# Performance work log

Hardware: AMD Instinct MI355X
Metric: run time of the kernel (lower is better)

## Reference

```python
import jax, jax.numpy as jnp
import numpy as np
import math

B, C, IMG, E, H, L, FF, D, NCLS = 4, 3, 64, 256, 8, 512, 4, 4, 1000
N = IMG * IMG  # 4096 pixel tokens
HS = H * E    # head_size = embedding_size * heads (per original code)


def setup_inputs() -> dict:
    key = jax.random.key(0)
    ks = jax.random.split(key, 32)
    s = 0.02
    nrm = lambda k, shape: (jax.random.normal(k, shape, jnp.float32) * s)
    inp = {
        "x": jax.random.normal(ks[0], (B, C, N), jnp.float32),
        "conv_w": nrm(ks[1], (E, C)),                 # 1x1 conv1d kernel
        "conv_b": jnp.zeros((E,), jnp.float32),
        "pos_emb": nrm(ks[2], (N, E)),
        "latents": jax.random.normal(ks[3], (L, E), jnp.float32),
        # cross-attention (queries from latents, keys/values from image tokens)
        "ca_wq": nrm(ks[4], (E, HS)),
        "ca_wk": nrm(ks[5], (E, HS)),
        "ca_wv": nrm(ks[6], (E, HS)),
        "ca_wu": nrm(ks[7], (HS, E)),
        "ca_bu": jnp.zeros((E,), jnp.float32),
        "ca_ln_g": jnp.ones((E,), jnp.float32),
        "ca_ln_b": jnp.zeros((E,), jnp.float32),
        # transformer blocks, stacked along depth for lax.scan
        "blk_wq": nrm(ks[8], (D, E, HS)),
        "blk_wk": nrm(ks[9], (D, E, HS)),
        "blk_wv": nrm(ks[10], (D, E, HS)),
        "blk_wu": nrm(ks[11], (D, HS, E)),
        "blk_bu": jnp.zeros((D, E), jnp.float32),
        "blk_ln1_g": jnp.ones((D, E), jnp.float32),
        "blk_ln1_b": jnp.zeros((D, E), jnp.float32),
        "blk_w1": nrm(ks[12], (D, E, FF * E)),
        "blk_b1": jnp.zeros((D, FF * E), jnp.float32),
        "blk_w2": nrm(ks[13], (D, FF * E, E)),
        "blk_b2": jnp.zeros((D, E), jnp.float32),
        "blk_ln2_g": jnp.ones((D, E), jnp.float32),
        "blk_ln2_b": jnp.zeros((D, E), jnp.float32),
        "cls_w": nrm(ks[14], (E, NCLS)),
        "cls_b": jnp.zeros((NCLS,), jnp.float32),
        "heads": H,
    }
    return inp


def _ln(x, g, b):
    m = jnp.mean(x, axis=-1, keepdims=True)
    v = jnp.mean(jnp.square(x - m), axis=-1, keepdims=True)
    return g * (x - m) * jax.lax.rsqrt(v + 1e-5) + b


def _mha(q_in, kv_in, wq, wk, wv, wu, bu, heads):
    # Faithful to original: each head has dim = embedding_size (head_size = heads*emb),
    # and the scale is sqrt(emb // heads).
    b, nq, e = q_in.shape
    nk = kv_in.shape[1]
    q = (q_in @ wq).reshape(b, nq, heads, e)
    k = (kv_in @ wk).reshape(b, nk, heads, e)
    v = (kv_in @ wv).reshape(b, nk, heads, e)
    scale = 1.0 / math.sqrt(e // heads)
    w = jax.nn.softmax(jnp.einsum('bqhe,bkhe->bhqk', q, k) * scale, axis=-1)
    a = jnp.einsum('bhqk,bkhe->bqhe', w, v).reshape(b, nq, heads * e)
    return a @ wu + bu


def reference(x, conv_w, conv_b, pos_emb, latents,
              ca_wq, ca_wk, ca_wv, ca_wu, ca_bu, ca_ln_g, ca_ln_b,
              blk_wq, blk_wk, blk_wv, blk_wu, blk_bu,
              blk_ln1_g, blk_ln1_b, blk_w1, blk_b1, blk_w2, blk_b2,
              blk_ln2_g, blk_ln2_b, cls_w, cls_b, heads):
    bsz = x.shape[0]
    # 1x1 conv1d over flattened pixels: (B, C, N) -> (B, N, E), plus positions
    tokens = jnp.einsum('bcn,ec->bne', x, conv_w) + conv_b + pos_emb
    # latents as queries, image tokens as keys/values (cross-attention)
    z = jnp.broadcast_to(latents, (bsz,) + latents.shape)
    z = _ln(_mha(z, tokens, ca_wq, ca_wk, ca_wv, ca_wu, ca_bu, heads) + z,
            ca_ln_g, ca_ln_b)
    # dropout is identity in eval mode

    def block(z, p):
        wq, wk, wv, wu, bu, g1, b1, w1, c1, w2, c2, g2, b2 = p
        z = _ln(_mha(z, z, wq, wk, wv, wu, bu, heads) + z, g1, b1)
        h = jax.nn.gelu(z @ w1 + c1, approximate=False) @ w2 + c2
        z = _ln(h + z, g2, b2)
        return z, None

    z, _ = jax.lax.scan(block, z,
                        (blk_wq, blk_wk, blk_wv, blk_wu, blk_bu,
                         blk_ln1_g, blk_ln1_b, blk_w1, blk_b1,
                         blk_w2, blk_b2, blk_ln2_g, blk_ln2_b))
    # global average over latents, then classifier
    return jnp.mean(z, axis=1) @ cls_w + cls_b
```

## Files before the change

### kernel.cpp

```cpp
#include <hip/hip_runtime.h>
#include <hip/hip_bf16.h>
#include <math.h>


typedef __attribute__((ext_vector_type(8))) short s8v;
typedef __attribute__((ext_vector_type(4))) float f32x4;
typedef __attribute__((ext_vector_type(16))) float f32x16;
typedef __attribute__((ext_vector_type(4))) unsigned u32x4;

__device__ __forceinline__ short f2b(float f) {
  union { float f; unsigned u; } a; a.f = f;
  unsigned r = a.u + 0x7fff + ((a.u >> 16) & 1);
  return (short)(r >> 16);
}
__device__ __forceinline__ float b2f(short s) {
  union { unsigned u; float f; } a; a.u = ((unsigned)(unsigned short)s) << 16;
  return a.f;
}
__device__ __forceinline__ unsigned cvtpk(float lo, float hi) {
  unsigned r;
  asm("v_cvt_pk_bf16_f32 %0, %1, %2" : "=v"(r) : "v"(lo), "v"(hi));
  return r;
}

__device__ __forceinline__ void gl16(const void* gp, void* lp) {
  __builtin_amdgcn_global_load_lds(
      (const __attribute__((address_space(1))) unsigned int*)gp,
      (__attribute__((address_space(3))) unsigned int*)lp, 16, 0, 0);
}

__global__ __launch_bounds__(256) void k_tokens(
    const float* __restrict__ x, const float* __restrict__ cw,
    const float* __restrict__ cb, const float* __restrict__ pe,
    short* __restrict__ tok)
{
  int idx = blockIdx.x * 256 + threadIdx.x;
  int e = idx & 255;
  int n = (idx >> 8) & 4095;
  int b = idx >> 20;
  float s = cb[e] + pe[n * 256 + e];
#pragma unroll
  for (int c = 0; c < 3; ++c)
    s += x[b * 12288 + c * 4096 + n] * cw[e * 3 + c];
  tok[idx] = f2b(s);
}

template<typename TI>
__global__ __launch_bounds__(256) void k_tr(
    const TI* __restrict__ in, short* __restrict__ out,
    int R, int C, long sIn, long sOut)
{
  __shared__ float t[32][33];
  const TI* ib = in + (long)blockIdx.z * sIn;
  short* ob = out + (long)blockIdx.z * sOut;
  int c0 = blockIdx.x * 32, r0 = blockIdx.y * 32;
  int tx = threadIdx.x & 31, ty = threadIdx.x >> 5;
#pragma unroll
  for (int i = 0; i < 4; ++i)
    t[ty * 4 + i][tx] = (float)ib[(long)(r0 + ty * 4 + i) * C + c0 + tx];
  __syncthreads();
#pragma unroll
  for (int i = 0; i < 4; ++i)
    ob[(long)(c0 + ty * 4 + i) * R + r0 + tx] = f2b(t[tx][ty * 4 + i]);
}

struct TrJob {
  const float* src; short* dst;
  int R, C; long sIn, sOut;
  int mode, tilesPerZ, z, tileBase;
  float scale;
};
struct TrJobs { TrJob j[11]; };

__global__ __launch_bounds__(256) void k_trbatch(TrJobs jb, int njobs)
{
  __shared__ float t[32][33];
  int tb = blockIdx.x, ji = 0;
#pragma unroll
  for (int k = 1; k < 11; ++k)
    if (k < njobs && tb >= jb.j[k].tileBase) ji = k;
  TrJob J = jb.j[ji];
  int local = tb - J.tileBase;
  if (J.mode == 1) {
    long o = (long)local * 8192 + threadIdx.x;
#pragma unroll
    for (int k = 0; k < 32; ++k)
      J.dst[o + k * 256] = f2b(J.src[o + k * 256] * J.scale);
    return;
  }
  int zi = local / J.tilesPerZ, ti = local - zi * J.tilesPerZ;
  int ntx = J.C >> 5;
  int tx = ti % ntx, ty = ti / ntx;
  const float* ib = J.src + (long)zi * J.sIn;
  short* ob = J.dst + (long)zi * J.sOut;
  int c0 = tx * 32, r0 = ty * 32;
  int lx = threadIdx.x & 31, ly = threadIdx.x >> 5;
#pragma unroll
  for (int i = 0; i < 4; ++i)
    t[ly * 4 + i][lx] = ib[(long)(r0 + ly * 4 + i) * J.C + c0 + lx];
  __syncthreads();
#pragma unroll
  for (int i = 0; i < 4; ++i)
    ob[(long)(c0 + ly * 4 + i) * J.R + r0 + lx] = f2b(t[lx][ly * 4 + i] * J.scale);
}

template<int EPI>
__global__ __launch_bounds__(256) void k_mgemm(
    const short* __restrict__ A, const short* __restrict__ Bt,
    void* __restrict__ Cv, const float* __restrict__ bias,
    int K, int lda, int ldb, int ldc,
    long sA, long sB, long sC, int zdA, int zmA, int zdB, int zmB)
{
  __shared__ char As[8192];
  __shared__ char Bs[8192];
  int z = blockIdx.z;
  const short* Ab = A + ((long)((z / zdA) % zmA)) * sA;
  const short* Bb = Bt + ((long)((z / zdB) % zmB)) * sB;
  int t = threadIdx.x;
  int lane = t & 63, w = t >> 6;
  int wr = w >> 1, wc = w & 1;
  int g = lane >> 4, l15 = lane & 15;
  long row0 = (long)blockIdx.y * 128, col0 = (long)blockIdx.x * 128;
  const f32x4 zz = {0.f, 0.f, 0.f, 0.f};
  f32x4 acc[4][4];
#pragma unroll
  for (int m = 0; m < 4; ++m)
#pragma unroll
    for (int n = 0; n < 4; ++n) acc[m][n] = zz;

  auto mload = [&](s8v* aa, s8v* bb, int kk) {
#pragma unroll
    for (int i = 0; i < 2; ++i) {
      int r = i * 64 + (t >> 2), c = t & 3;
      aa[i] = *(const s8v*)&Ab[(row0 + r) * (long)lda + kk + c * 8];
      bb[i] = *(const s8v*)&Bb[(col0 + r) * (long)ldb + kk + c * 8];
    }
  };
  auto mstore = [&](s8v* aa, s8v* bb) {
#pragma unroll
    for (int i = 0; i < 2; ++i) {
      int r = i * 64 + (t >> 2), c = t & 3;
      int off = (r * 64 + c * 16) ^ ((r & 7) << 4);
      *(s8v*)&As[off] = aa[i];
      *(s8v*)&Bs[off] = bb[i];
    }
  };
  auto mcomp = [&]() {
    s8v af[4], bfr[4];
#pragma unroll
    for (int m = 0; m < 4; ++m) {
      int r = wr * 64 + m * 16 + l15;
      af[m] = *(const s8v*)&As[(r * 64 + g * 16) ^ ((r & 7) << 4)];
    }
#pragma unroll
    for (int n = 0; n < 4; ++n) {
      int r = wc * 64 + n * 16 + l15;
      bfr[n] = *(const s8v*)&Bs[(r * 64 + g * 16) ^ ((r & 7) << 4)];
    }
#pragma unroll
    for (int m = 0; m < 4; ++m)
#pragma unroll
      for (int n = 0; n < 4; ++n)
        acc[m][n] = __builtin_amdgcn_mfma_f32_16x16x32_bf16(af[m], bfr[n], acc[m][n], 0, 0, 0);
  };

  s8v a0[2], b0[2], a1[2], b1[2];
  mload(a0, b0, 0);
  for (int k0 = 0; k0 < K; k0 += 64) {
    __syncthreads(); mstore(a0, b0); __syncthreads();
    mload(a1, b1, k0 + 32);
    mcomp();
    __syncthreads(); mstore(a1, b1); __syncthreads();
    if (k0 + 64 < K) mload(a0, b0, k0 + 64);
    mcomp();
  }

  long zo = (long)z * sC;
#pragma unroll
  for (int m = 0; m < 4; ++m)
#pragma unroll
    for (int n = 0; n < 4; ++n)
#pragma unroll
      for (int r = 0; r < 4; ++r) {
        long rr = row0 + wr * 64 + m * 16 + g * 4 + r;
        long cc = col0 + wc * 64 + n * 16 + l15;
        float v = acc[m][n][r];
        if (EPI == 1) {
          v += bias[cc];
          v = 0.5f * v * (1.f + erff(v * 0.70710678118654752f));
        }
        if (EPI == 2)
          ((float*)Cv)[zo + rr * ldc + cc] = v;
        else
          ((short*)Cv)[zo + rr * ldc + cc] = f2b(v);
      }
}

__global__ __launch_bounds__(512, 2) void k_mflash5(
    const short* __restrict__ Qp, const short* __restrict__ Kp,
    const short* __restrict__ Vtp, short* __restrict__ Opart,
    float* __restrict__ MLp,
    int nk, int ldq, int ldk, int ldvt,
    long qh, long qb, long kh, long kb, long vh, long vb)
{
  __shared__ char pool[131072];
  int t = threadIdx.x, lane = t & 63, w = t >> 6;
  int l31 = lane & 31, hi = lane >> 5;
  int h = blockIdx.y, b = blockIdx.z;
  int kv = blockIdx.x & 3, qblk = blockIdx.x >> 2;
  const short* Q  = Qp  + (long)h * qh + (long)b * qb;
  const short* Kg = Kp  + (long)h * kh + (long)b * kb;
  const short* Vg = Vtp + (long)h * vh + (long)b * vb;
  int q0w = qblk * 256 + w * 32;
  int nkq = nk >> 2;
  int NIT = nkq >> 6;
  long k0 = (long)kv * nkq;

  s8v qf[16];
  {
    const short* Qrow = Q + (long)(q0w + l31) * ldq + hi * 8;
#pragma unroll
    for (int s = 0; s < 16; ++s) qf[s] = *(const s8v*)(Qrow + s * 16);
  }

  const char* KgB = (const char*)Kg;
  const char* VgB = (const char*)Vg;
  unsigned koff[4], voff[4];
#pragma unroll
  for (int c = 0; c < 4; ++c) {
    int r = 8 * w + 2 * c + hi;
    koff[c] = (unsigned)((k0 + r) * (long)ldk * 2) + ((l31 ^ (r & 31)) << 4);
    int rv = 32 * w + 8 * c + (lane >> 3);
    voff[c] = (unsigned)(((long)rv * ldvt + k0) * 2) + (((lane & 7) ^ (lane >> 3)) << 4);
  }
  const unsigned kStep = (unsigned)(64 * ldk * 2);

  auto stage = [&](int bsel) {
    char* kd = pool + bsel * 65536 + (w << 12);
    char* vd = kd + 32768;
#pragma unroll
    for (int c = 0; c < 4; ++c) { gl16(KgB + koff[c], kd + c * 1024); koff[c] += kStep; }
#pragma unroll
    for (int c = 0; c < 4; ++c) { gl16(VgB + voff[c], vd + c * 1024); voff[c] += 128; }
  };

  f32x16 accO[8];
#pragma unroll
  for (int n = 0; n < 8; ++n)
#pragma unroll
    for (int i = 0; i < 16; ++i) accO[n][i] = 0.f;
  float mrow = -1e30f, lrow = 0.f;

  stage(0);

  for (int it = 0; it < NIT; ++it) {
    int cur = it & 1;
    asm volatile("s_waitcnt vmcnt(0)" ::: "memory");
    __syncthreads();
    if (it + 1 < NIT) stage(cur ^ 1);
    const char* kls = pool + cur * 65536;
    const char* vls = kls + 32768;

    f32x16 sacc[2];
#pragma unroll
    for (int i = 0; i < 16; ++i) { sacc[0][i] = 0.f; sacc[1][i] = 0.f; }
    __builtin_amdgcn_s_setprio(1);
#pragma unroll
    for (int tt = 0; tt < 2; ++tt) {
      int r = tt * 32 + l31;
#pragma unroll
      for (int s = 0; s < 16; ++s) {
        s8v kf = *(const s8v*)&kls[r * 512 + (((2 * s + hi) ^ l31) << 4)];
        sacc[tt] = __builtin_amdgcn_mfma_f32_32x32x16_bf16(kf, qf[s], sacc[tt], 0, 0, 0);
      }
    }
    __builtin_amdgcn_s_setprio(0);

    float mt = sacc[0][0];
#pragma unroll
    for (int i = 1; i < 16; ++i) mt = fmaxf(mt, sacc[0][i]);
#pragma unroll
    for (int i = 0; i < 16; ++i) mt = fmaxf(mt, sacc[1][i]);
    mt = fmaxf(mt, __shfl_xor(mt, 32));
    if (__any(mt - mrow > 8.f)) {
      float mn = fmaxf(mrow, mt);
      float al = __expf(mrow - mn);
      mrow = mn; lrow *= al;
#pragma unroll
      for (int r = 0; r < 16; ++r) {
        float alr = __shfl(al, (r & 3) + 8 * (r >> 2) + 4 * hi);
#pragma unroll
        for (int n = 0; n < 8; ++n) accO[n][r] *= alr;
      }
    }
    float ls = 0.f;
#pragma unroll
    for (int tt = 0; tt < 2; ++tt)
#pragma unroll
      for (int i = 0; i < 16; ++i) {
        float p = __expf(sacc[tt][i] - mrow);
        sacc[tt][i] = p; ls += p;
      }
    ls += __shfl_xor(ls, 32);
    lrow += ls;

    s8v pa[4];
#pragma unroll
    for (int s = 0; s < 4; ++s) {
      int tt = s >> 1, r0 = (s & 1) * 8;
      unsigned w0 = cvtpk(sacc[tt][r0 + 0], sacc[tt][r0 + 1]);
      unsigned w1 = cvtpk(sacc[tt][r0 + 2], sacc[tt][r0 + 3]);
      unsigned w2 = cvtpk(sacc[tt][r0 + 4], sacc[tt][r0 + 5]);
      unsigned w3 = cvtpk(sacc[tt][r0 + 6], sacc[tt][r0 + 7]);
      unsigned x0 = (unsigned)__shfl_xor((int)w0, 32);
      unsigned x1 = (unsigned)__shfl_xor((int)w1, 32);
      unsigned x2 = (unsigned)__shfl_xor((int)w2, 32);
      unsigned x3 = (unsigned)__shfl_xor((int)w3, 32);
      u32x4 pw;
      pw.x = hi ? x2 : w0;
      pw.y = hi ? x3 : w1;
      pw.z = hi ? w2 : x0;
      pw.w = hi ? w3 : x1;
      pa[s] = *(s8v*)&pw;
    }

    __builtin_amdgcn_s_setprio(1);
#pragma unroll
    for (int n = 0; n < 8; ++n) {
      int rv = n * 32 + l31;
#pragma unroll
      for (int s2 = 0; s2 < 4; ++s2) {
        s8v vf = *(const s8v*)&vls[rv * 128 + (((2 * s2 + hi) ^ (l31 & 7)) << 4)];
        accO[n] = __builtin_amdgcn_mfma_f32_32x32x16_bf16(pa[s2], vf, accO[n], 0, 0, 0);
      }
    }
    __builtin_amdgcn_s_setprio(0);
  }

  long prow = (((long)kv * 4 + b) * 8 + h) * 512;
  short* Ob = Opart + prow * 256;
  float* MLb = MLp + prow * 2;
  if (lane < 32) {
    MLb[(q0w + l31) * 2] = mrow;
    MLb[(q0w + l31) * 2 + 1] = lrow;
  }
#pragma unroll
  for (int n = 0; n < 8; ++n)
#pragma unroll
    for (int r = 0; r < 16; ++r) {
      int q = q0w + (r & 3) + 8 * (r >> 2) + 4 * hi;
      Ob[(long)q * 256 + n * 32 + l31] = f2b(accO[n][r]);
    }
}

__global__ __launch_bounds__(512) void k_fcomb(
    const short* __restrict__ Op, const float* __restrict__ ML,
    short* __restrict__ O)
{
  int d = threadIdx.x & 255;
  int q = blockIdx.x * 2 + (threadIdx.x >> 8);
  int h = blockIdx.y, b = blockIdx.z;
  const long kvs = 4L * 8 * 512;
  long r0 = ((long)b * 8 + h) * 512 + q;
  float mm[4], ll[4], m = -1e30f;
#pragma unroll
  for (int kv = 0; kv < 4; ++kv) {
    mm[kv] = ML[(kv * kvs + r0) * 2];
    ll[kv] = ML[(kv * kvs + r0) * 2 + 1];
    m = fmaxf(m, mm[kv]);
  }
  float wv[4], lsum = 0.f;
#pragma unroll
  for (int kv = 0; kv < 4; ++kv) { wv[kv] = __expf(mm[kv] - m); lsum += ll[kv] * wv[kv]; }
  float inv = 1.f / lsum, acc = 0.f;
#pragma unroll
  for (int kv = 0; kv < 4; ++kv)
    acc += b2f(Op[(kv * kvs + r0) * 256 + d]) * wv[kv];
  O[(long)b * 1048576 + (long)q * 2048 + h * 256 + d] = f2b(acc * inv);
}

__global__ __launch_bounds__(256) void k_bias_res_ln(
    const float* __restrict__ Yp, int nPart, long pStride,
    const float* __restrict__ bias,
    const float* __restrict__ res, int resMod,
    const float* __restrict__ g, const float* __restrict__ bta,
    float* __restrict__ out, short* __restrict__ out_bf)
{
  __shared__ float red[4];
  int row = blockIdx.x, e = threadIdx.x;
  float v = bias[e] + res[(long)(row % resMod) * 256 + e];
  for (int s = 0; s < nPart; ++s) v += Yp[s * pStride + (long)row * 256 + e];
  float s1 = v;
#pragma unroll
  for (int o = 32; o > 0; o >>= 1) s1 += __shfl_down(s1, o);
  if ((e & 63) == 0) red[e >> 6] = s1;
  __syncthreads();
  float mean = (red[0] + red[1] + red[2] + red[3]) * (1.f / 256.f);
  float d = v - mean;
  __syncthreads();
  float s2 = d * d;
#pragma unroll
  for (int o = 32; o > 0; o >>= 1) s2 += __shfl_down(s2, o);
  if ((e & 63) == 0) red[e >> 6] = s2;
  __syncthreads();
  float var = (red[0] + red[1] + red[2] + red[3]) * (1.f / 256.f);
  float o = g[e] * d * rsqrtf(var + 1e-5f) + bta[e];
  out[(long)row * 256 + e] = o;
  out_bf[(long)row * 256 + e] = f2b(o);
}

__global__ __launch_bounds__(256) void k_meancls(
    const float* __restrict__ z, const float* __restrict__ w,
    const float* __restrict__ bias, float* __restrict__ out)
{
  __shared__ float zms[256];
  int b = blockIdx.y, e = threadIdx.x;
  float s = 0.f;
  for (int l = 0; l < 512; ++l) s += z[((long)b * 512 + l) * 256 + e];
  zms[e] = s * (1.f / 512.f);
  __syncthreads();
  int j = blockIdx.x * 256 + e;
  if (j >= 1000) return;
  float acc = bias[j];
  for (int e2 = 0; e2 < 256; ++e2) acc += zms[e2] * w[e2 * 1000 + j];
  out[b * 1000 + j] = acc;
}

extern "C" void kernel_launch(void* const* d_in, const int* in_sizes, int n_in,
                              void* d_out, int out_size, void* d_ws, size_t ws_size,
                              hipStream_t stream)
{
  (void)in_sizes; (void)n_in; (void)out_size; (void)ws_size;
  const float* x       = (const float*)d_in[0];
  const float* conv_w  = (const float*)d_in[1];
  const float* conv_b  = (const float*)d_in[2];
  const float* pos_emb = (const float*)d_in[3];
  const float* latents = (const float*)d_in[4];
  const float* ca_wq   = (const float*)d_in[5];
  const float* ca_wk   = (const float*)d_in[6];
  const float* ca_wv   = (const float*)d_in[7];
  const float* ca_wu   = (const float*)d_in[8];
  const float* ca_bu   = (const float*)d_in[9];
  const float* ca_ln_g = (const float*)d_in[10];
  const float* ca_ln_b = (const float*)d_in[11];
  const float* blk_wq  = (const float*)d_in[12];
  const float* blk_wk  = (const float*)d_in[13];
  const float* blk_wv  = (const float*)d_in[14];
  const float* blk_wu  = (const float*)d_in[15];
  const float* blk_bu  = (const float*)d_in[16];
  const float* blk_ln1_g = (const float*)d_in[17];
  const float* blk_ln1_b = (const float*)d_in[18];
  const float* blk_w1  = (const float*)d_in[19];
  const float* blk_b1  = (const float*)d_in[20];
  const float* blk_w2  = (const float*)d_in[21];
  const float* blk_b2  = (const float*)d_in[22];
  const float* blk_ln2_g = (const float*)d_in[23];
  const float* blk_ln2_b = (const float*)d_in[24];
  const float* cls_w   = (const float*)d_in[25];
  const float* cls_b   = (const float*)d_in[26];
  float* out = (float*)d_out;

  short* wqT_ca = (short*)d_ws;
  short* wkT_ca = wqT_ca + 524288;
  short* wuT_ca = wkT_ca + 524288;
  short* wv_ca  = wuT_ca + 524288;
  short* lat_bf = wv_ca + 524288;
  short* wqkT   = lat_bf + 131072;
  short* wvT    = wqkT + 4194304;
  short* wuT_b  = wvT + 2097152;
  short* w1T    = wuT_b + 2097152;
  short* w2T    = w1T + 1048576;
  short* tok_bf = w2T + 1048576;
  short* tokT   = tok_bf + 4194304;
  short* qCA    = tokT + 4194304;
  short* qtil   = qCA + 1048576;
  short* MstT   = qtil + 1048576;
  short* VtB    = MstT + 524288;
  short* bufO   = VtB + 4194304;
  short* h1     = bufO + 4194304;
  short* z_bf   = h1 + 2097152;
  float* z      = (float*)(z_bf + 524288);
  float* zm     = z + 524288;
  float* Ypart  = zm + 1024;
  short* Opart  = (short*)(Ypart + 4194304);
  float* MLp    = (float*)(Opart + 16777216);
  short* QKb    = tok_bf;

  const float scale = 0.17677669529663687f;
  const int BIG = 1 << 30;

  TrJobs JB; int nj = 0, base = 0;
  auto addT = [&](const float* s, short* d, int R, int C, long sIn, long sOut,
                  int zc, float sc) {
    int tpz = (C >> 5) * (R >> 5);
    JB.j[nj] = {s, d, R, C, sIn, sOut, 0, tpz, zc, base, sc};
    base += tpz * zc; ++nj;
  };
  auto addC = [&](const float* s, short* d, int nelem) {
    int tpz = nelem >> 13;
    JB.j[nj] = {s, d, 0, 0, 0, 0, 1, tpz, 1, base, 1.f};
    base += tpz; ++nj;
  };
  addT(ca_wq, wqT_ca, 256, 2048, 0, 0, 1, scale);
  addT(ca_wk, wkT_ca, 256, 2048, 0, 0, 1, 1.f);
  addT(ca_wu, wuT_ca, 2048, 256, 0, 0, 1, 1.f);
  addT(blk_wq, wqkT, 256, 2048, 524288, 1048576, 4, scale);
  addT(blk_wk, wqkT + 524288, 256, 2048, 524288, 1048576, 4, 1.f);
  addT(blk_wv, wvT, 256, 2048, 524288, 524288, 4, 1.f);
  addT(blk_wu, wuT_b, 2048, 256, 524288, 524288, 4, 1.f);
  addT(blk_w1, w1T, 256, 1024, 262144, 262144, 4, 1.f);
  addT(blk_w2, w2T, 1024, 256, 262144, 262144, 4, 1.f);
  addC(ca_wv, wv_ca, 524288);
  addC(latents, lat_bf, 131072);
  k_trbatch<<<base, 256, 0, stream>>>(JB, nj);

  k_tokens<<<16384, 256, 0, stream>>>(x, conv_w, conv_b, pos_emb, tok_bf);
  k_tr<__hip_bfloat16><<<dim3(8, 128, 4), 256, 0, stream>>>(
      (const __hip_bfloat16*)tok_bf, tokT, 4096, 256, 1048576, 1048576);

  k_mgemm<0><<<dim3(16, 4, 1), 256, 0, stream>>>(
      lat_bf, wqT_ca, qCA, nullptr, 256, 256, 256, 2048, 0, 0, 0, 1, BIG, 1, BIG);
  k_mgemm<0><<<dim3(2, 4, 8), 256, 0, stream>>>(
      qCA, wkT_ca, qtil, nullptr, 256, 2048, 256, 256, 256, 65536, 131072, 1, 8, 1, 8);
  k_mgemm<0><<<dim3(2, 2, 8), 256, 0, stream>>>(
      wuT_ca, wv_ca, MstT, nullptr, 256, 2048, 2048, 2048, 256, 256, 256, 1, 8, 1, 8);
  k_mflash5<<<dim3(8, 8, 4), 512, 0, stream>>>(
      qtil, tok_bf, tokT, Opart, MLp, 4096, 256, 256, 4096,
      131072L, 0L, 0L, 1048576L, 0L, 1048576L);
  k_fcomb<<<dim3(256, 8, 4), 512, 0, stream>>>(Opart, MLp, bufO);
  k_mgemm<2><<<dim3(2, 16, 8), 256, 0, stream>>>(
      bufO, MstT, Ypart, nullptr, 256, 2048, 2048, 256, 256, 256, 524288, 1, 8, 1, 8);
  k_bias_res_ln<<<2048, 256, 0, stream>>>(Ypart, 8, 524288L, ca_bu, latents, 512,
                                          ca_ln_g, ca_ln_b, z, z_bf);

  for (int d = 0; d < 4; ++d) {
    k_mgemm<0><<<dim3(32, 16, 1), 256, 0, stream>>>(
        z_bf, wqkT + (long)d * 1048576, QKb, nullptr,
        256, 256, 256, 4096, 0, 0, 0, 1, BIG, 1, BIG);
    k_mgemm<0><<<dim3(4, 2, 32), 256, 0, stream>>>(
        wvT + (long)d * 524288, z_bf, VtB, nullptr,
        256, 256, 256, 512, 65536, 131072, 131072, 1, 8, 8, BIG);
    k_mflash5<<<dim3(8, 8, 4), 512, 0, stream>>>(
        QKb, QKb + 2048, VtB, Opart, MLp, 512, 4096, 4096, 512,
        256L, 2097152L, 256L, 2097152L, 131072L, 1048576L);
    k_fcomb<<<dim3(256, 8, 4), 512, 0, stream>>>(Opart, MLp, bufO);
    k_mgemm<2><<<dim3(2, 16, 8), 256, 0, stream>>>(
        bufO, wuT_b + (long)d * 524288, Ypart, nullptr,
        256, 2048, 2048, 256, 256, 256, 524288, 1, 8, 1, 8);
    k_bias_res_ln<<<2048, 256, 0, stream>>>(Ypart, 8, 524288L, blk_bu + d * 256, z, 2048,
        blk_ln1_g + d * 256, blk_ln1_b + d * 256, z, z_bf);
    k_mgemm<1><<<dim3(8, 16, 1), 256, 0, stream>>>(
        z_bf, w1T + (long)d * 262144, h1, blk_b1 + d * 1024,
        256, 256, 256, 1024, 0, 0, 0, 1, BIG, 1, BIG);
    k_mgemm<2><<<dim3(2, 16, 8), 256, 0, stream>>>(
        h1, w2T + (long)d * 262144, Ypart, nullptr,
        128, 1024, 1024, 256, 128, 128, 524288, 1, 8, 1, 8);
    k_bias_res_ln<<<2048, 256, 0, stream>>>(Ypart, 8, 524288L, blk_b2 + d * 256, z, 2048,
        blk_ln2_g + d * 256, blk_ln2_b + d * 256, z, z_bf);
  }

  k_meancls<<<dim3(4, 4), 256, 0, stream>>>(z, cls_w, cls_b, out);
}
```

Before: 635.7 us.

## Batch GEMMs into multi-job launches, fuse token transpose, refine flash waits

Replaces the templated GEMM with a job-table kernel so independent GEMMs (QK and V projections, cross-attention weight products) share one launch. Token embedding now writes both the row-major and the transposed copy, which removes a separate transpose kernel. The cross-attention Wq·Wk product is now computed from weights first, dropping the latent Q projection. The flash kernel uses partial vmcnt waits plus an extra barrier so K loads overlap the softmax. The epilogue mode becomes a runtime branch, and the transposed token stores are uncoalesced strided writes.

```diff
diff --git a/kernel.cpp b/kernel.cpp
--- a/kernel.cpp
+++ b/kernel.cpp
@@ -29,39 +29,27 @@
       (__attribute__((address_space(3))) unsigned int*)lp, 16, 0, 0);
 }
 
-__global__ __launch_bounds__(256) void k_tokens(
+__global__ __launch_bounds__(256) void k_tokens2(
     const float* __restrict__ x, const float* __restrict__ cw,
     const float* __restrict__ cb, const float* __restrict__ pe,
-    short* __restrict__ tok)
-{
-  int idx = blockIdx.x * 256 + threadIdx.x;
-  int e = idx & 255;
-  int n = (idx >> 8) & 4095;
-  int b = idx >> 20;
-  float s = cb[e] + pe[n * 256 + e];
-#pragma unroll
-  for (int c = 0; c < 3; ++c)
-    s += x[b * 12288 + c * 4096 + n] * cw[e * 3 + c];
-  tok[idx] = f2b(s);
-}
-
-template<typename TI>
-__global__ __launch_bounds__(256) void k_tr(
-    const TI* __restrict__ in, short* __restrict__ out,
-    int R, int C, long sIn, long sOut)
-{
-  __shared__ float t[32][33];
-  const TI* ib = in + (long)blockIdx.z * sIn;
-  short* ob = out + (long)blockIdx.z * sOut;
-  int c0 = blockIdx.x * 32, r0 = blockIdx.y * 32;
-  int tx = threadIdx.x & 31, ty = threadIdx.x >> 5;
-#pragma unroll
-  for (int i = 0; i < 4; ++i)
-    t[ty * 4 + i][tx] = (float)ib[(long)(r0 + ty * 4 + i) * C + c0 + tx];
-  __syncthreads();
-#pragma unroll
-  for (int i = 0; i < 4; ++i)
-    ob[(long)(c0 + ty * 4 + i) * R + r0 + tx] = f2b(t[tx][ty * 4 + i]);
+    short* __restrict__ tok, short* __restrict__ tokT)
+{
+  int b = blockIdx.y, n0 = blockIdx.x * 32;
+  int e = threadIdx.x;
+  float c0 = cw[e * 3], c1 = cw[e * 3 + 1], c2 = cw[e * 3 + 2], cbv = cb[e];
+  const float* xb = x + b * 12288 + n0;
+  short acc[32];
+#pragma unroll
+  for (int i = 0; i < 32; ++i) {
+    int n = n0 + i;
+    float s = cbv + pe[n * 256 + e] + xb[i] * c0 + xb[4096 + i] * c1 + xb[8192 + i] * c2;
+    short v = f2b(s);
+    tok[((long)b * 4096 + n) * 256 + e] = v;
+    acc[i] = v;
+  }
+  short* tr = tokT + ((long)b * 256 + e) * 4096 + n0;
+#pragma unroll
+  for (int i = 0; i < 32; ++i) tr[i] = acc[i];
 }
 
 struct TrJob {
@@ -104,23 +92,35 @@
     ob[(long)(c0 + ly * 4 + i) * J.R + r0 + lx] = f2b(t[lx][ly * 4 + i] * J.scale);
 }
 
-template<int EPI>
-__global__ __launch_bounds__(256) void k_mgemm(
-    const short* __restrict__ A, const short* __restrict__ Bt,
-    void* __restrict__ Cv, const float* __restrict__ bias,
-    int K, int lda, int ldb, int ldc,
-    long sA, long sB, long sC, int zdA, int zmA, int zdB, int zmB)
+struct GJob {
+  const short* A; const short* Bt; void* C; const float* bias;
+  int K, lda, ldb, ldc;
+  long sA, sB, sC;
+  int zdA, zmA, zdB, zmB;
+  int epi, gx, gy, blockBase;
+};
+struct GJobs { GJob j[4]; };
+
+__global__ __launch_bounds__(256) void k_gemm_m(GJobs jb, int njobs)
 {
   __shared__ char As[8192];
   __shared__ char Bs[8192];
-  int z = blockIdx.z;
-  const short* Ab = A + ((long)((z / zdA) % zmA)) * sA;
-  const short* Bb = Bt + ((long)((z / zdB) % zmB)) * sB;
+  int bid = blockIdx.x, ji = 0;
+#pragma unroll
+  for (int k = 1; k < 4; ++k)
+    if (k < njobs && bid >= jb.j[k].blockBase) ji = k;
+  GJob J = jb.j[ji];
+  int local = bid - J.blockBase;
+  int bx = local % J.gx, rest = local / J.gx;
+  int by = rest % J.gy, bz = rest / J.gy;
+  const short* Ab = J.A + ((long)((bz / J.zdA) % J.zmA)) * J.sA;
+  const short* Bb = J.Bt + ((long)((bz / J.zdB) % J.zmB)) * J.sB;
+  int lda = J.lda, ldb = J.ldb;
   int t = threadIdx.x;
   int lane = t & 63, w = t >> 6;
   int wr = w >> 1, wc = w & 1;
   int g = lane >> 4, l15 = lane & 15;
-  long row0 = (long)blockIdx.y * 128, col0 = (long)blockIdx.x * 128;
+  long row0 = (long)by * 128, col0 = (long)bx * 128;
   const f32x4 zz = {0.f, 0.f, 0.f, 0.f};
   f32x4 acc[4][4];
 #pragma unroll
@@ -166,16 +166,16 @@
 
   s8v a0[2], b0[2], a1[2], b1[2];
   mload(a0, b0, 0);
-  for (int k0 = 0; k0 < K; k0 += 64) {
+  for (int k0 = 0; k0 < J.K; k0 += 64) {
     __syncthreads(); mstore(a0, b0); __syncthreads();
     mload(a1, b1, k0 + 32);
     mcomp();
     __syncthreads(); mstore(a1, b1); __syncthreads();
-    if (k0 + 64 < K) mload(a0, b0, k0 + 64);
+    if (k0 + 64 < J.K) mload(a0, b0, k0 + 64);
     mcomp();
   }
 
-  long zo = (long)z * sC;
+  long zo = (long)bz * J.sC;
 #pragma unroll
   for (int m = 0; m < 4; ++m)
 #pragma unroll
@@ -185,18 +185,18 @@
         long rr = row0 + wr * 64 + m * 16 + g * 4 + r;
         long cc = col0 + wc * 64 + n * 16 + l15;
         float v = acc[m][n][r];
-        if (EPI == 1) {
-          v += bias[cc];
+        if (J.epi == 1) {
+          v += J.bias[cc];
           v = 0.5f * v * (1.f + erff(v * 0.70710678118654752f));
         }
-        if (EPI == 2)
-          ((float*)Cv)[zo + rr * ldc + cc] = v;
+        if (J.epi == 2)
+          ((float*)J.C)[zo + rr * J.ldc + cc] = v;
         else
-          ((short*)Cv)[zo + rr * ldc + cc] = f2b(v);
+          ((short*)J.C)[zo + rr * J.ldc + cc] = f2b(v);
       }
 }
 
-__global__ __launch_bounds__(512, 2) void k_mflash5(
+__global__ __launch_bounds__(512, 2) void k_mflash6(
     const short* __restrict__ Qp, const short* __restrict__ Kp,
     const short* __restrict__ Vtp, short* __restrict__ Opart,
     float* __restrict__ MLp,
@@ -255,7 +255,7 @@
 
   for (int it = 0; it < NIT; ++it) {
     int cur = it & 1;
-    asm volatile("s_waitcnt vmcnt(0)" ::: "memory");
+    asm volatile("s_waitcnt vmcnt(4)" ::: "memory");
     __syncthreads();
     if (it + 1 < NIT) stage(cur ^ 1);
     const char* kls = pool + cur * 65536;
@@ -323,6 +323,10 @@
       pw.w = hi ? w3 : x1;
       pa[s] = *(s8v*)&pw;
     }
+
+    if (it + 1 < NIT) { asm volatile("s_waitcnt vmcnt(8)" ::: "memory"); }
+    else              { asm volatile("s_waitcnt vmcnt(0)" ::: "memory"); }
+    __syncthreads();
 
     __builtin_amdgcn_s_setprio(1);
 #pragma unroll
@@ -460,9 +464,9 @@
   const float* cls_b   = (const float*)d_in[26];
   float* out = (float*)d_out;
 
-  short* wqT_ca = (short*)d_ws;
-  short* wkT_ca = wqT_ca + 524288;
-  short* wuT_ca = wkT_ca + 524288;
+  short* wq_bf  = (short*)d_ws;
+  short* wk_bf  = wq_bf + 524288;
+  short* wuT_ca = wk_bf + 524288;
   short* wv_ca  = wuT_ca + 524288;
   short* lat_bf = wv_ca + 524288;
   short* wqkT   = lat_bf + 131072;
@@ -472,22 +476,21 @@
   short* w2T    = w1T + 1048576;
   short* tok_bf = w2T + 1048576;
   short* tokT   = tok_bf + 4194304;
-  short* qCA    = tokT + 4194304;
-  short* qtil   = qCA + 1048576;
+  short* WqkT   = tokT + 4194304;
+  short* qtil   = WqkT + 524288;
   short* MstT   = qtil + 1048576;
   short* VtB    = MstT + 524288;
   short* bufO   = VtB + 4194304;
   short* h1     = bufO + 4194304;
   short* z_bf   = h1 + 2097152;
   float* z      = (float*)(z_bf + 524288);
-  float* zm     = z + 524288;
-  float* Ypart  = zm + 1024;
+  float* Ypart  = z + 524288;
   short* Opart  = (short*)(Ypart + 4194304);
   float* MLp    = (float*)(Opart + 16777216);
   short* QKb    = tok_bf;
+  const int BIG = 1 << 30;
 
   const float scale = 0.17677669529663687f;
-  const int BIG = 1 << 30;
 
   TrJobs JB; int nj = 0, base = 0;
   auto addT = [&](const float* s, short* d, int R, int C, long sIn, long sOut,
@@ -496,13 +499,11 @@
     JB.j[nj] = {s, d, R, C, sIn, sOut, 0, tpz, zc, base, sc};
     base += tpz * zc; ++nj;
   };
-  auto addC = [&](const float* s, short* d, int nelem) {
+  auto addC = [&](const float* s, short* d, int nelem, float sc) {
     int tpz = nelem >> 13;
-    JB.j[nj] = {s, d, 0, 0, 0, 0, 1, tpz, 1, base, 1.f};
+    JB.j[nj] = {s, d, 0, 0, 0, 0, 1, tpz, 1, base, sc};
     base += tpz; ++nj;
   };
-  addT(ca_wq, wqT_ca, 256, 2048, 0, 0, 1, scale);
-  addT(ca_wk, wkT_ca, 256, 2048, 0, 0, 1, 1.f);
   addT(ca_wu, wuT_ca, 2048, 256, 0, 0, 1, 1.f);
   addT(blk_wq, wqkT, 256, 2048, 524288, 1048576, 4, scale);
   addT(blk_wk, wqkT + 524288, 256, 2048, 524288, 1048576, 4, 1.f);
@@ -510,51 +511,76 @@
   addT(blk_wu, wuT_b, 2048, 256, 524288, 524288, 4, 1.f);
   addT(blk_w1, w1T, 256, 1024, 262144, 262144, 4, 1.f);
   addT(blk_w2, w2T, 1024, 256, 262144, 262144, 4, 1.f);
-  addC(ca_wv, wv_ca, 524288);
-  addC(latents, lat_bf, 131072);
+  addC(ca_wv, wv_ca, 524288, 1.f);
+  addC(latents, lat_bf, 131072, 1.f);
+  addC(ca_wq, wq_bf, 524288, scale);
+  addC(ca_wk, wk_bf, 524288, 1.f);
   k_trbatch<<<base, 256, 0, stream>>>(JB, nj);
 
-  k_tokens<<<16384, 256, 0, stream>>>(x, conv_w, conv_b, pos_emb, tok_bf);
-  k_tr<__hip_bfloat16><<<dim3(8, 128, 4), 256, 0, stream>>>(
-      (const __hip_bfloat16*)tok_bf, tokT, 4096, 256, 1048576, 1048576);
-
-  k_mgemm<0><<<dim3(16, 4, 1), 256, 0, stream>>>(
-      lat_bf, wqT_ca, qCA, nullptr, 256, 256, 256, 2048, 0, 0, 0, 1, BIG, 1, BIG);
-  k_mgemm<0><<<dim3(2, 4, 8), 256, 0, stream>>>(
-      qCA, wkT_ca, qtil, nullptr, 256, 2048, 256, 256, 256, 65536, 131072, 1, 8, 1, 8);
-  k_mgemm<0><<<dim3(2, 2, 8), 256, 0, stream>>>(
-      wuT_ca, wv_ca, MstT, nullptr, 256, 2048, 2048, 2048, 256, 256, 256, 1, 8, 1, 8);
-  k_mflash5<<<dim3(8, 8, 4), 512, 0, stream>>>(
+  k_tokens2<<<dim3(128, 4), 256, 0, stream>>>(x, conv_w, conv_b, pos_emb,
+                                              tok_bf, tokT);
+
+  {
+    GJobs G;
+    G.j[0] = {wk_bf, wq_bf, WqkT, nullptr, 256, 2048, 2048, 256,
+              256, 256, 65536, 1, 8, 1, 8, 0, 2, 2, 0};
+    G.j[1] = {wuT_ca, wv_ca, MstT, nullptr, 256, 2048, 2048, 2048,
+              256, 256, 256, 1, 8, 1, 8, 0, 2, 2, 32};
+    k_gemm_m<<<64, 256, 0, stream>>>(G, 2);
+  }
+  {
+    GJobs G;
+    G.j[0] = {lat_bf, WqkT, qtil, nullptr, 256, 256, 256, 256,
+              0, 65536, 131072, 1, 1, 1, 8, 0, 2, 4, 0};
+    k_gemm_m<<<64, 256, 0, stream>>>(G, 1);
+  }
+  k_mflash6<<<dim3(8, 8, 4), 512, 0, stream>>>(
       qtil, tok_bf, tokT, Opart, MLp, 4096, 256, 256, 4096,
       131072L, 0L, 0L, 1048576L, 0L, 1048576L);
   k_fcomb<<<dim3(256, 8, 4), 512, 0, stream>>>(Opart, MLp, bufO);
-  k_mgemm<2><<<dim3(2, 16, 8), 256, 0, stream>>>(
-      bufO, MstT, Ypart, nullptr, 256, 2048, 2048, 256, 256, 256, 524288, 1, 8, 1, 8);
+  {
+    GJobs G;
+    G.j[0] = {bufO, MstT, Ypart, nullptr, 256, 2048, 2048, 256,
+              256, 256, 524288, 1, 8, 1, 8, 2, 2, 16, 0};
+    k_gemm_m<<<256, 256, 0, stream>>>(G, 1);
+  }
   k_bias_res_ln<<<2048, 256, 0, stream>>>(Ypart, 8, 524288L, ca_bu, latents, 512,
                                           ca_ln_g, ca_ln_b, z, z_bf);
 
   for (int d = 0; d < 4; ++d) {
-    k_mgemm<0><<<dim3(32, 16, 1), 256, 0, stream>>>(
-        z_bf, wqkT + (long)d * 1048576, QKb, nullptr,
-        256, 256, 256, 4096, 0, 0, 0, 1, BIG, 1, BIG);
-    k_mgemm<0><<<dim3(4, 2, 32), 256, 0, stream>>>(
-        wvT + (long)d * 524288, z_bf, VtB, nullptr,
-        256, 256, 256, 512, 65536, 131072, 131072, 1, 8, 8, BIG);
-    k_mflash5<<<dim3(8, 8, 4), 512, 0, stream>>>(
+    {
+      GJobs G;
+      G.j[0] = {z_bf, wqkT + (long)d * 1048576, QKb, nullptr,
+                256, 256, 256, 4096, 0, 0, 0, 1, 1, 1, 1, 0, 32, 16, 0};
+      G.j[1] = {wvT + (long)d * 524288, z_bf, VtB, nullptr,
+                256, 256, 256, 512, 65536, 131072, 131072,
+                1, 8, 8, BIG, 0, 4, 2, 512};
+      k_gemm_m<<<768, 256, 0, stream>>>(G, 2);
+    }
+    k_mflash6<<<dim3(8, 8, 4), 512, 0, stream>>>(
         QKb, QKb + 2048, VtB, Opart, MLp, 512, 4096, 4096, 512,
         256L, 2097152L, 256L, 2097152L, 131072L, 1048576L);
     k_fcomb<<<dim3(256, 8, 4), 512, 0, stream>>>(Opart, MLp, bufO);
-    k_mgemm<2><<<dim3(2, 16, 8), 256, 0, stream>>>(
-        bufO, wuT_b + (long)d * 524288, Ypart, nullptr,
-        256, 2048, 2048, 256, 256, 256, 524288, 1, 8, 1, 8);
+    {
+      GJobs G;
+      G.j[0] = {bufO, wuT_b + (long)d * 524288, Ypart, nullptr,
+                256, 2048, 2048, 256, 256, 256, 524288, 1, 8, 1, 8, 2, 2, 16, 0};
+      k_gemm_m<<<256, 256, 0, stream>>>(G, 1);
+    }
     k_bias_res_ln<<<2048, 256, 0, stream>>>(Ypart, 8, 524288L, blk_bu + d * 256, z, 2048,
         blk_ln1_g + d * 256, blk_ln1_b + d * 256, z, z_bf);
-    k_mgemm<1><<<dim3(8, 16, 1), 256, 0, stream>>>(
-        z_bf, w1T + (long)d * 262144, h1, blk_b1 + d * 1024,
-        256, 256, 256, 1024, 0, 0, 0, 1, BIG, 1, BIG);
-    k_mgemm<2><<<dim3(2, 16, 8), 256, 0, stream>>>(
-        h1, w2T + (long)d * 262144, Ypart, nullptr,
-        128, 1024, 1024, 256, 128, 128, 524288, 1, 8, 1, 8);
+    {
+      GJobs G;
+      G.j[0] = {z_bf, w1T + (long)d * 262144, h1, blk_b1 + d * 1024,
+                256, 256, 256, 1024, 0, 0, 0, 1, 1, 1, 1, 1, 8, 16, 0};
+      k_gemm_m<<<128, 256, 0, stream>>>(G, 1);
+    }
+    {
+      GJobs G;
+      G.j[0] = {h1, w2T + (long)d * 262144, Ypart, nullptr,
+                128, 1024, 1024, 256, 128, 128, 524288, 1, 8, 1, 8, 2, 2, 16, 0};
+      k_gemm_m<<<256, 256, 0, stream>>>(G, 1);
+    }
     k_bias_res_ln<<<2048, 256, 0, stream>>>(Ypart, 8, 524288L, blk_b2 + d * 256, z, 2048,
         blk_ln2_g + d * 256, blk_ln2_b + d * 256, z, z_bf);
   }
```

After: 695.8 us. 1.09x slower.
